# Kernel tuning notes

Hardware: AMD Instinct MI355X
Metric: run time of the kernel (lower is better)

Reference implementation:

```python
import jax, jax.numpy as jnp
import numpy as np

NUM_HEADS = 32
ROPE_BASE = 10000.0
MASK_NEG = -66504.0  # from (1 - tril) * -66504.0 in the source


def _rotate_half(x):
    d = x.shape[-1] // 2
    return jnp.concatenate([-x[..., d:], x[..., :d]], axis=-1)


def setup_inputs() -> dict:
    key = jax.random.key(0)
    k1, k2, k3, k4 = jax.random.split(key, 4)
    S, B, E = 2048, 2, 2048
    return {
        "hidden_states": jax.random.normal(k1, (S, B, E), dtype=jnp.float32) * 0.02,
        "qkv_w": jax.random.normal(k2, (E, 3 * E), dtype=jnp.float32) * 0.02,
        "qkv_b": jax.random.normal(k3, (3 * E,), dtype=jnp.float32) * 0.02,
        "out_w": jax.random.normal(k4, (E, E), dtype=jnp.float32) * 0.02,
        "out_b": jnp.zeros((E,), dtype=jnp.float32),
    }


def reference(hidden_states, qkv_w, qkv_b, out_w, out_b):
    # seq-first prompt/prefill path of IPEXTransformerAtten
    S, B, E = hidden_states.shape
    H = NUM_HEADS
    D = E // H

    # fused QKV projection (mm_qkv_out)
    qkv = jnp.einsum('sbe,ef->sbf', hidden_states, qkv_w) + qkv_b  # [S,B,3E]
    q, k, v = jnp.split(qkv, 3, axis=-1)
    q = q.reshape(S, B, H, D)
    k = k.reshape(S, B, H, D)
    v = v.reshape(S, B, H, D)

    # rotary embedding (GPT-NeoX style, full head_dim)
    inv_freq = 1.0 / (ROPE_BASE ** (jnp.arange(0, D, 2, dtype=jnp.float32) / D))
    freqs = jnp.arange(S, dtype=jnp.float32)[:, None] * inv_freq  # [S, D/2]
    emb = jnp.concatenate([freqs, freqs], axis=-1)  # [S, D]
    cos = jnp.cos(emb)[:, None, None, :].astype(hidden_states.dtype)
    sin = jnp.sin(emb)[:, None, None, :].astype(hidden_states.dtype)
    q = q * cos + _rotate_half(q) * sin
    k = k * cos + _rotate_half(k) * sin

    # scaled dot-product attention with causal mask
    scale = 1.0 / jnp.sqrt(jnp.array(D, dtype=hidden_states.dtype))
    scores = jnp.einsum('sbhd,tbhd->bhst', q, k) * scale  # [B,H,S,S]
    causal = jnp.tril(jnp.ones((S, S), dtype=scores.dtype))
    scores = scores + (1.0 - causal) * MASK_NEG
    attn = jax.nn.softmax(scores, axis=-1)
    ctx = jnp.einsum('bhst,tbhd->sbhd', attn, v).reshape(S, B, E)

    # output projection
    return jnp.einsum('sbe,ef->sbf', ctx, out_w) + out_b
```

## Files before the change

kernel.cpp:

```cpp
#include <hip/hip_runtime.h>
#include <hip/hip_bf16.h>

#define S_LEN 2048
#define BATCH 2
#define EMB   2048
#define NH    32
#define HD    64
#define M_ROWS (S_LEN * BATCH)
#define QKV_N  (3 * EMB)

typedef short bf16x8 __attribute__((ext_vector_type(8)));
typedef float f32x4  __attribute__((ext_vector_type(4)));

__device__ __forceinline__ unsigned short f2bf(float f) {
  unsigned int u = __float_as_uint(f);
  u += 0x7fffu + ((u >> 16) & 1u);
  return (unsigned short)(u >> 16);
}
__device__ __forceinline__ float bf2f(unsigned short h) {
  return __uint_as_float(((unsigned int)h) << 16);
}
__device__ __forceinline__ void async_copy16(const void* g, void* lds) {
  __builtin_amdgcn_global_load_lds(
      (const __attribute__((address_space(1))) void*)g,
      (__attribute__((address_space(3))) void*)lds, 16, 0, 0);
}

#if __has_builtin(__builtin_amdgcn_exp2f)
#define EXP2F(x) __builtin_amdgcn_exp2f(x)
#else
#define EXP2F(x) __expf((x) * 0.6931471805599453f)
#endif


__global__ __launch_bounds__(256) void cast_to_bf16(
    const float* __restrict__ in, unsigned short* __restrict__ out, int n4) {
  int i = blockIdx.x * 256 + threadIdx.x;
  if (i >= n4) return;
  float4 v = reinterpret_cast<const float4*>(in)[i];
  ushort4 o;
  o.x = f2bf(v.x); o.y = f2bf(v.y); o.z = f2bf(v.z); o.w = f2bf(v.w);
  reinterpret_cast<ushort4*>(out)[i] = o;
}

__global__ __launch_bounds__(256) void transpose_cast(
    const float* __restrict__ in, unsigned short* __restrict__ out, int R, int C) {
  __shared__ float tile[32][33];
  const int bc = blockIdx.x * 32, br = blockIdx.y * 32;
  const int tx = threadIdx.x & 31, ty = threadIdx.x >> 5;
  #pragma unroll
  for (int rr = ty; rr < 32; rr += 8)
    tile[rr][tx] = in[(size_t)(br + rr) * C + bc + tx];
  __syncthreads();
  #pragma unroll
  for (int rr = ty; rr < 32; rr += 8)
    out[(size_t)(bc + rr) * R + br + tx] = f2bf(tile[tx][rr]);
}


__global__ __launch_bounds__(256) void gemm_qkv(
    const unsigned short* __restrict__ A,
    const unsigned short* __restrict__ Wt,
    const float* __restrict__ bias,
    unsigned short* __restrict__ Qo,
    unsigned short* __restrict__ Ko,
    unsigned short* __restrict__ Vo) {
  __shared__ __align__(16) unsigned short As[128 * 64];
  __shared__ __align__(16) unsigned short Bs[128 * 64];
  const int tid = threadIdx.x;
  const int n0 = blockIdx.x * 128;
  const int m0 = blockIdx.y * 128;
  const int wave = tid >> 6, lane = tid & 63;
  const int wm = (wave >> 1) * 64, wn = (wave & 1) * 64;
  const int lm = lane & 15, lq = lane >> 4;
  const int K = 2048;

  const int srow = tid >> 3;
  const int gch  = (tid & 7) ^ (srow & 7);
  const unsigned short* Ab = A  + (size_t)(m0 + srow) * K + gch * 8;
  const unsigned short* Bb = Wt + (size_t)(n0 + srow) * K + gch * 8;

  f32x4 acc[4][4] = {};

  for (int k0 = 0; k0 < K; k0 += 64) {
    #pragma unroll
    for (int rep = 0; rep < 4; rep++) {
      async_copy16(Ab + (size_t)rep * 32 * K + k0, As + (size_t)(tid + 256 * rep) * 8);
      async_copy16(Bb + (size_t)rep * 32 * K + k0, Bs + (size_t)(tid + 256 * rep) * 8);
    }
    __syncthreads();
    #pragma unroll
    for (int ks = 0; ks < 2; ks++) {
      bf16x8 a[4], b[4];
      #pragma unroll
      for (int i = 0; i < 4; i++) {
        const int R = wm + i*16 + lm;
        a[i] = *reinterpret_cast<const bf16x8*>(
            As + (size_t)R * 64 + (((ks*4 + lq) ^ (R & 7)) * 8));
      }
      #pragma unroll
      for (int j = 0; j < 4; j++) {
        const int R = wn + j*16 + lm;
        b[j] = *reinterpret_cast<const bf16x8*>(
            Bs + (size_t)R * 64 + (((ks*4 + lq) ^ (R & 7)) * 8));
      }
      #pragma unroll
      for (int i = 0; i < 4; i++)
        #pragma unroll
        for (int j = 0; j < 4; j++)
          acc[i][j] = __builtin_amdgcn_mfma_f32_16x16x32_bf16(a[i], b[j], acc[i][j], 0, 0, 0);
    }
    __syncthreads();
  }

  const int which = n0 >> 11;
  unsigned short* dst = (which == 0) ? Qo : (which == 1) ? Ko : Vo;
  float bv[4];
  #pragma unroll
  for (int j = 0; j < 4; j++) bv[j] = bias[n0 + wn + j*16 + lm];

  if (which < 2) {
    #pragma unroll
    for (int j = 0; j < 2; j++) {
      const int n = n0 + wn + j*16 + lm;
      const int e = n & (EMB - 1), h = e >> 6, d = e & 63;
      const float invf = EXP2F((float)d * -0.4152410118609203f);
      #pragma unroll
      for (int i = 0; i < 4; i++) {
        #pragma unroll
        for (int r = 0; r < 4; r++) {
          const int m = m0 + wm + i*16 + lq*4 + r;
          const int s = m >> 1, b = m & 1;
          const float v1 = acc[i][j][r]   + bv[j];
          const float v2 = acc[i][j+2][r] + bv[j+2];
          float sn, cs;
          __sincosf((float)s * invf, &sn, &cs);
          const size_t base = (((size_t)b * NH + h) * S_LEN + s) * HD + d;
          dst[base]      = f2bf(v1 * cs - v2 * sn);
          dst[base + 32] = f2bf(v2 * cs + v1 * sn);
        }
      }
    }
  } else {
    #pragma unroll
    for (int j = 0; j < 4; j++) {
      const int n = n0 + wn + j*16 + lm;
      const int e = n & (EMB - 1), h = e >> 6, d = e & 63;
      #pragma unroll
      for (int i = 0; i < 4; i++) {
        #pragma unroll
        for (int r = 0; r < 4; r++) {
          const int m = m0 + wm + i*16 + lq*4 + r;
          const int s = m >> 1, b = m & 1;
          dst[(((size_t)b * NH + h) * S_LEN + s) * HD + d] = f2bf(acc[i][j][r] + bv[j]);
        }
      }
    }
  }
}


__global__ __launch_bounds__(256) void transpose_v(
    const unsigned short* __restrict__ V, unsigned short* __restrict__ VT) {
  __shared__ unsigned short t[64][65];
  const int bh = blockIdx.y;
  const int s0 = blockIdx.x * 64;
  const int tx = threadIdx.x & 63, ty = threadIdx.x >> 6;
  const unsigned short* src = V + ((size_t)bh * S_LEN + s0) * HD;
  #pragma unroll
  for (int r = ty; r < 64; r += 4)
    t[r][tx] = src[(size_t)r * HD + tx];
  __syncthreads();
  unsigned short* dst = VT + (size_t)bh * HD * S_LEN + s0;
  #pragma unroll
  for (int r = ty; r < 64; r += 4)
    dst[(size_t)r * S_LEN + tx] = t[tx][r];
}


__global__ __launch_bounds__(256) void attn_kernel(
    const unsigned short* __restrict__ Q,
    const unsigned short* __restrict__ K,
    const unsigned short* __restrict__ VT,
    unsigned short* __restrict__ ctx) {
  const int bh = blockIdx.x;
  const int p  = blockIdx.y;
  const int tid = threadIdx.x;
  const int wave = tid >> 6, lane = tid & 63;
  const int lm = lane & 15, lq = lane >> 4;
  const int b = bh >> 5, h = bh & 31;
  const char* Qb8 = (const char*)(Q  + (size_t)bh * S_LEN * HD);
  const char* Kb8 = (const char*)(K  + (size_t)bh * S_LEN * HD);
  const char* Vb8 = (const char*)(VT + (size_t)bh * HD * S_LEN);

  __shared__ __align__(16) unsigned short Ks[2][2][64][32];
  __shared__ __align__(16) unsigned short Vs[2][2][64][32];
  __shared__ __align__(16) unsigned short Pbuf[4][32][72];
  unsigned short* Pw = &Pbuf[wave][0][0];

  const float C = 0.18033688011112042f;
  const int q0A = p * 128, q0B = (15 - p) * 128;
  const int r0A = q0A + wave * 32, r0B = q0B + wave * 32;
  const int nt = (q0B >> 6) + 2;

  const int srw = tid >> 2, sc16 = (tid & 3) * 16;

  bf16x8 qf[2][2][2];
  #pragma unroll
  for (int s = 0; s < 2; s++) {
    const int rr = (s == 0) ? r0A : r0B;
    #pragma unroll
    for (int i = 0; i < 2; i++)
      #pragma unroll
      for (int ks = 0; ks < 2; ks++)
        qf[s][i][ks] = *reinterpret_cast<const bf16x8*>(
            Qb8 + (size_t)(rr + i*16 + lm) * 128 + ks*64 + lq*16);
  }

  f32x4 O[2][2][4] = {};
  float l[2][2][4] = {};

  {
    char* kd = (char*)&Ks[0][0][0][0];
    char* vd = (char*)&Vs[0][0][0][0];
    async_copy16(Kb8 + (size_t)srw * 128      + sc16, kd        + tid*16);
    async_copy16(Kb8 + (size_t)srw * 128 + 64 + sc16, kd + 4096 + tid*16);
    async_copy16(Vb8 + (size_t)srw * 4096      + sc16, vd        + tid*16);
    async_copy16(Vb8 + (size_t)srw * 4096 + 64 + sc16, vd + 4096 + tid*16);
  }
  __syncthreads();

  for (int t = 0; t < nt; t++) {
    const int t0 = t * 64;
    const int buf = t & 1;

    if (t + 1 < nt) {
      const int t1 = t0 + 64;
      char* kd = (char*)&Ks[buf ^ 1][0][0][0];
      char* vd = (char*)&Vs[buf ^ 1][0][0][0];
      async_copy16(Kb8 + (size_t)(t1 + srw) * 128      + sc16, kd        + tid*16);
      async_copy16(Kb8 + (size_t)(t1 + srw) * 128 + 64 + sc16, kd + 4096 + tid*16);
      async_copy16(Vb8 + (size_t)srw * 4096 + t1*2      + sc16, vd        + tid*16);
      async_copy16(Vb8 + (size_t)srw * 4096 + t1*2 + 64 + sc16, vd + 4096 + tid*16);
    }

    const char* KsB = (const char*)&Ks[buf][0][0][0];
    const char* VsB = (const char*)&Vs[buf][0][0][0];

    #pragma unroll
    for (int s = 0; s < 2; s++) {
      const int rr = (s == 0) ? r0A : r0B;
      if (t0 <= rr + 31) {
        const bool clean = (t0 + 63 <= rr);
        const int jmax  = clean ? 4 : ((rr == t0) ? 2 : 4);
        const int kslim = clean ? 2 : ((rr == t0) ? 1 : 2);
        const int srow_c = rr + lq * 4;

        f32x4 sc[2][4] = {};
        #pragma unroll
        for (int ks = 0; ks < 2; ks++) {
          bf16x8 kf[4];
          #pragma unroll
          for (int j = 0; j < 4; j++)
            if (j < jmax)
              kf[j] = *reinterpret_cast<const bf16x8*>(
                  KsB + ks*4096 + (j*16 + lm)*64 + lq*16);
          #pragma unroll
          for (int i = 0; i < 2; i++)
            #pragma unroll
            for (int j = 0; j < 4; j++)
              if (j < jmax)
                sc[i][j] = __builtin_amdgcn_mfma_f32_16x16x32_bf16(
                    qf[s][i][ks], kf[j], sc[i][j], 0, 0, 0);
        }

        if (clean) {
          #pragma unroll
          for (int i = 0; i < 2; i++)
            #pragma unroll
            for (int j = 0; j < 4; j++)
              #pragma unroll
              for (int r = 0; r < 4; r++) {
                const float pe = EXP2F(sc[i][j][r] * C);
                l[s][i][r] += pe;
                Pw[(i*16 + lq*4 + r) * 72 + j*16 + lm] = f2bf(pe);
              }
        } else {
          #pragma unroll
          for (int i = 0; i < 2; i++)
            #pragma unroll
            for (int j = 0; j < 4; j++)
              if (j < jmax)
                #pragma unroll
                for (int r = 0; r < 4; r++) {
                  const int srow = srow_c + i*16 + r;
                  const int tcol = t0 + j*16 + lm;
                  const float pe = (tcol <= srow) ? EXP2F(sc[i][j][r] * C) : 0.0f;
                  l[s][i][r] += pe;
                  Pw[(i*16 + lq*4 + r) * 72 + j*16 + lm] = f2bf(pe);
                }
        }

        #pragma unroll
        for (int ks = 0; ks < 2; ks++) {
          if (ks < kslim) {
            bf16x8 pf[2], vf[4];
            #pragma unroll
            for (int i = 0; i < 2; i++)
              pf[i] = *reinterpret_cast<const bf16x8*>(Pw + (i*16 + lm)*72 + ks*32 + lq*8);
            #pragma unroll
            for (int j = 0; j < 4; j++)
              vf[j] = *reinterpret_cast<const bf16x8*>(
                  VsB + ks*4096 + (j*16 + lm)*64 + lq*16);
            #pragma unroll
            for (int i = 0; i < 2; i++)
              #pragma unroll
              for (int j = 0; j < 4; j++)
                O[s][i][j] = __builtin_amdgcn_mfma_f32_16x16x32_bf16(
                    pf[i], vf[j], O[s][i][j], 0, 0, 0);
          }
        }
      }
    }
    __syncthreads();
  }

  #pragma unroll
  for (int s = 0; s < 2; s++) {
    const int rr = (s == 0) ? r0A : r0B;
    #pragma unroll
    for (int i = 0; i < 2; i++) {
      #pragma unroll
      for (int r = 0; r < 4; r++) {
        float sum = l[s][i][r];
        sum += __shfl_xor(sum, 1, 64);
        sum += __shfl_xor(sum, 2, 64);
        sum += __shfl_xor(sum, 4, 64);
        sum += __shfl_xor(sum, 8, 64);
        const float inv = 1.0f / sum;
        const int srow = rr + lq*4 + i*16 + r;
        #pragma unroll
        for (int j = 0; j < 4; j++) {
          const int d = j*16 + lm;
          ctx[((size_t)srow * BATCH + b) * EMB + h*HD + d] = f2bf(O[s][i][j][r] * inv);
        }
      }
    }
  }
}


__global__ __launch_bounds__(256) void gemm_out(
    const unsigned short* __restrict__ A,
    const unsigned short* __restrict__ Wt,
    const float* __restrict__ bias,
    float* __restrict__ out) {
  __shared__ __align__(16) unsigned short As[128 * 64];
  __shared__ __align__(16) unsigned short Bs[128 * 64];
  const int tid = threadIdx.x;
  const int n0 = blockIdx.x * 128;
  const int m0 = blockIdx.y * 128;
  const int wave = tid >> 6, lane = tid & 63;
  const int wm = (wave >> 1) * 64, wn = (wave & 1) * 64;
  const int lm = lane & 15, lq = lane >> 4;
  const int K = 2048;

  const int srow = tid >> 3;
  const int gch  = (tid & 7) ^ (srow & 7);
  const unsigned short* Ab = A  + (size_t)(m0 + srow) * K + gch * 8;
  const unsigned short* Bb = Wt + (size_t)(n0 + srow) * K + gch * 8;

  f32x4 acc[4][4] = {};

  for (int k0 = 0; k0 < K; k0 += 64) {
    #pragma unroll
    for (int rep = 0; rep < 4; rep++) {
      async_copy16(Ab + (size_t)rep * 32 * K + k0, As + (size_t)(tid + 256 * rep) * 8);
      async_copy16(Bb + (size_t)rep * 32 * K + k0, Bs + (size_t)(tid + 256 * rep) * 8);
    }
    __syncthreads();
    #pragma unroll
    for (int ks = 0; ks < 2; ks++) {
      bf16x8 a[4], b[4];
      #pragma unroll
      for (int i = 0; i < 4; i++) {
        const int R = wm + i*16 + lm;
        a[i] = *reinterpret_cast<const bf16x8*>(
            As + (size_t)R * 64 + (((ks*4 + lq) ^ (R & 7)) * 8));
      }
      #pragma unroll
      for (int j = 0; j < 4; j++) {
        const int R = wn + j*16 + lm;
        b[j] = *reinterpret_cast<const bf16x8*>(
            Bs + (size_t)R * 64 + (((ks*4 + lq) ^ (R & 7)) * 8));
      }
      #pragma unroll
      for (int i = 0; i < 4; i++)
        #pragma unroll
        for (int j = 0; j < 4; j++)
          acc[i][j] = __builtin_amdgcn_mfma_f32_16x16x32_bf16(a[i], b[j], acc[i][j], 0, 0, 0);
    }
    __syncthreads();
  }

  #pragma unroll
  for (int j = 0; j < 4; j++) {
    const int n = n0 + wn + j*16 + lm;
    const float bv = bias[n];
    #pragma unroll
    for (int i = 0; i < 4; i++) {
      #pragma unroll
      for (int r = 0; r < 4; r++) {
        const int m = m0 + wm + i*16 + lq*4 + r;
        out[(size_t)m * EMB + n] = acc[i][j][r] + bv;
      }
    }
  }
}


extern "C" void kernel_launch(void* const* d_in, const int* in_sizes, int n_in,
                              void* d_out, int out_size, void* d_ws, size_t ws_size,
                              hipStream_t stream) {
  const float* hidden = (const float*)d_in[0];
  const float* qkv_w  = (const float*)d_in[1];
  const float* qkv_b  = (const float*)d_in[2];
  const float* out_w  = (const float*)d_in[3];
  const float* out_b  = (const float*)d_in[4];
  float* out = (float*)d_out;

  unsigned short* ws = (unsigned short*)d_ws;
  unsigned short* hbf   = ws;
  unsigned short* qkvwT = hbf   + (size_t)M_ROWS * EMB;
  unsigned short* outwT = qkvwT + (size_t)QKV_N * EMB;
  unsigned short* Qb    = outwT + (size_t)EMB * EMB;
  unsigned short* Kb    = Qb    + (size_t)64 * S_LEN * HD;
  unsigned short* Vb    = Kb    + (size_t)64 * S_LEN * HD;
  unsigned short* VTb   = Vb    + (size_t)64 * S_LEN * HD;
  unsigned short* ctx   = VTb   + (size_t)64 * S_LEN * HD;

  cast_to_bf16<<<(M_ROWS * EMB / 4) / 256, 256, 0, stream>>>(hidden, hbf, M_ROWS * EMB / 4);
  transpose_cast<<<dim3(QKV_N / 32, EMB / 32), 256, 0, stream>>>(qkv_w, qkvwT, EMB, QKV_N);
  transpose_cast<<<dim3(EMB / 32, EMB / 32), 256, 0, stream>>>(out_w, outwT, EMB, EMB);

  gemm_qkv<<<dim3(QKV_N / 128, M_ROWS / 128), 256, 0, stream>>>(hbf, qkvwT, qkv_b, Qb, Kb, Vb);

  transpose_v<<<dim3(S_LEN / 64, 64), 256, 0, stream>>>(Vb, VTb);

  attn_kernel<<<dim3(64, 8), 256, 0, stream>>>(Qb, Kb, VTb, ctx);

  gemm_out<<<dim3(EMB / 128, M_ROWS / 128), 256, 0, stream>>>(ctx, outwT, out_b, out);
}
```

Before: 368.1 us.

## Halve attention query tile per block, double-buffer out GEMM, merge weight transposes

The attention kernel now gives each wave 16 query rows instead of 32 and launches twice as many blocks (64x16), still pairing a low and a high causal tile for load balance. This raises parallelism on the many-CU GPU and cuts per-wave registers, at the cost of reusing each K/V tile over fewer query rows. The output GEMM gains double-buffered LDS with async prefetch of the next K slice. The two weight transpose launches are merged into one 3D-grid launch.

```diff
diff --git a/kernel.cpp b/kernel.cpp
--- a/kernel.cpp
+++ b/kernel.cpp
@@ -43,10 +43,17 @@
   reinterpret_cast<ushort4*>(out)[i] = o;
 }
 
-__global__ __launch_bounds__(256) void transpose_cast(
-    const float* __restrict__ in, unsigned short* __restrict__ out, int R, int C) {
+__global__ __launch_bounds__(256) void transpose_cast2(
+    const float* __restrict__ qkv_w, const float* __restrict__ out_w,
+    unsigned short* __restrict__ qkvwT, unsigned short* __restrict__ outwT) {
   __shared__ float tile[32][33];
-  const int bc = blockIdx.x * 32, br = blockIdx.y * 32;
+  const int z = blockIdx.z;
+  const int C = z ? EMB : QKV_N;
+  const int bc = blockIdx.x * 32;
+  if (bc >= C) return;
+  const float* in = z ? out_w : qkv_w;
+  unsigned short* out = z ? outwT : qkvwT;
+  const int br = blockIdx.y * 32;
   const int tx = threadIdx.x & 31, ty = threadIdx.x >> 5;
   #pragma unroll
   for (int rr = ty; rr < 32; rr += 8)
@@ -54,7 +61,7 @@
   __syncthreads();
   #pragma unroll
   for (int rr = ty; rr < 32; rr += 8)
-    out[(size_t)(bc + rr) * R + br + tx] = f2bf(tile[tx][rr]);
+    out[(size_t)(bc + rr) * EMB + br + tx] = f2bf(tile[tx][rr]);
 }
 
 
@@ -195,30 +202,28 @@
 
   __shared__ __align__(16) unsigned short Ks[2][2][64][32];
   __shared__ __align__(16) unsigned short Vs[2][2][64][32];
-  __shared__ __align__(16) unsigned short Pbuf[4][32][72];
+  __shared__ __align__(16) unsigned short Pbuf[4][16][72];
   unsigned short* Pw = &Pbuf[wave][0][0];
 
   const float C = 0.18033688011112042f;
-  const int q0A = p * 128, q0B = (15 - p) * 128;
-  const int r0A = q0A + wave * 32, r0B = q0B + wave * 32;
-  const int nt = (q0B >> 6) + 2;
+  const int rA = p * 64 + wave * 16;
+  const int rB = (31 - p) * 64 + wave * 16;
+  const int nt = 32 - p;
 
   const int srw = tid >> 2, sc16 = (tid & 3) * 16;
 
-  bf16x8 qf[2][2][2];
+  bf16x8 qf[2][2];
   #pragma unroll
   for (int s = 0; s < 2; s++) {
-    const int rr = (s == 0) ? r0A : r0B;
-    #pragma unroll
-    for (int i = 0; i < 2; i++)
-      #pragma unroll
-      for (int ks = 0; ks < 2; ks++)
-        qf[s][i][ks] = *reinterpret_cast<const bf16x8*>(
-            Qb8 + (size_t)(rr + i*16 + lm) * 128 + ks*64 + lq*16);
-  }
-
-  f32x4 O[2][2][4] = {};
-  float l[2][2][4] = {};
+    const int rr = (s == 0) ? rA : rB;
+    #pragma unroll
+    for (int ks = 0; ks < 2; ks++)
+      qf[s][ks] = *reinterpret_cast<const bf16x8*>(
+          Qb8 + (size_t)(rr + lm) * 128 + ks*64 + lq*16);
+  }
+
+  f32x4 O[2][4] = {};
+  float l[2][4] = {};
 
   {
     char* kd = (char*)&Ks[0][0][0][0];
@@ -249,14 +254,13 @@
 
     #pragma unroll
     for (int s = 0; s < 2; s++) {
-      const int rr = (s == 0) ? r0A : r0B;
-      if (t0 <= rr + 31) {
+      const int rr = (s == 0) ? rA : rB;
+      if (t0 <= rr + 15) {
         const bool clean = (t0 + 63 <= rr);
-        const int jmax  = clean ? 4 : ((rr == t0) ? 2 : 4);
-        const int kslim = clean ? 2 : ((rr == t0) ? 1 : 2);
-        const int srow_c = rr + lq * 4;
-
-        f32x4 sc[2][4] = {};
+        const int jmax = clean ? 4 : min(4, ((rr + 15 - t0) >> 4) + 1);
+        const int kslim = (jmax + 1) >> 1;
+
+        f32x4 sc[4] = {};
         #pragma unroll
         for (int ks = 0; ks < 2; ks++) {
           bf16x8 kf[4];
@@ -266,58 +270,53 @@
               kf[j] = *reinterpret_cast<const bf16x8*>(
                   KsB + ks*4096 + (j*16 + lm)*64 + lq*16);
           #pragma unroll
-          for (int i = 0; i < 2; i++)
-            #pragma unroll
-            for (int j = 0; j < 4; j++)
-              if (j < jmax)
-                sc[i][j] = __builtin_amdgcn_mfma_f32_16x16x32_bf16(
-                    qf[s][i][ks], kf[j], sc[i][j], 0, 0, 0);
+          for (int j = 0; j < 4; j++)
+            if (j < jmax)
+              sc[j] = __builtin_amdgcn_mfma_f32_16x16x32_bf16(
+                  qf[s][ks], kf[j], sc[j], 0, 0, 0);
         }
 
         if (clean) {
           #pragma unroll
-          for (int i = 0; i < 2; i++)
+          for (int j = 0; j < 4; j++)
             #pragma unroll
-            for (int j = 0; j < 4; j++)
+            for (int r = 0; r < 4; r++) {
+              const float pe = EXP2F(sc[j][r] * C);
+              l[s][r] += pe;
+              Pw[(lq*4 + r) * 72 + j*16 + lm] = f2bf(pe);
+            }
+        } else {
+          #pragma unroll
+          for (int j = 0; j < 4; j++)
+            if (j < jmax)
               #pragma unroll
               for (int r = 0; r < 4; r++) {
-                const float pe = EXP2F(sc[i][j][r] * C);
-                l[s][i][r] += pe;
-                Pw[(i*16 + lq*4 + r) * 72 + j*16 + lm] = f2bf(pe);
+                const int srow = rr + lq*4 + r;
+                const int tcol = t0 + j*16 + lm;
+                const float pe = (tcol <= srow) ? EXP2F(sc[j][r] * C) : 0.0f;
+                l[s][r] += pe;
+                Pw[(lq*4 + r) * 72 + j*16 + lm] = f2bf(pe);
               }
-        } else {
-          #pragma unroll
-          for (int i = 0; i < 2; i++)
+          if (jmax & 1) {
             #pragma unroll
-            for (int j = 0; j < 4; j++)
-              if (j < jmax)
-                #pragma unroll
-                for (int r = 0; r < 4; r++) {
-                  const int srow = srow_c + i*16 + r;
-                  const int tcol = t0 + j*16 + lm;
-                  const float pe = (tcol <= srow) ? EXP2F(sc[i][j][r] * C) : 0.0f;
-                  l[s][i][r] += pe;
-                  Pw[(i*16 + lq*4 + r) * 72 + j*16 + lm] = f2bf(pe);
-                }
+            for (int r = 0; r < 4; r++)
+              Pw[(lq*4 + r) * 72 + jmax*16 + lm] = 0;
+          }
         }
 
         #pragma unroll
         for (int ks = 0; ks < 2; ks++) {
           if (ks < kslim) {
-            bf16x8 pf[2], vf[4];
-            #pragma unroll
-            for (int i = 0; i < 2; i++)
-              pf[i] = *reinterpret_cast<const bf16x8*>(Pw + (i*16 + lm)*72 + ks*32 + lq*8);
+            bf16x8 pf = *reinterpret_cast<const bf16x8*>(Pw + lm*72 + ks*32 + lq*8);
+            bf16x8 vf[4];
             #pragma unroll
             for (int j = 0; j < 4; j++)
               vf[j] = *reinterpret_cast<const bf16x8*>(
                   VsB + ks*4096 + (j*16 + lm)*64 + lq*16);
             #pragma unroll
-            for (int i = 0; i < 2; i++)
-              #pragma unroll
-              for (int j = 0; j < 4; j++)
-                O[s][i][j] = __builtin_amdgcn_mfma_f32_16x16x32_bf16(
-                    pf[i], vf[j], O[s][i][j], 0, 0, 0);
+            for (int j = 0; j < 4; j++)
+              O[s][j] = __builtin_amdgcn_mfma_f32_16x16x32_bf16(
+                  pf, vf[j], O[s][j], 0, 0, 0);
           }
         }
       }
@@ -327,23 +326,20 @@
 
   #pragma unroll
   for (int s = 0; s < 2; s++) {
-    const int rr = (s == 0) ? r0A : r0B;
-    #pragma unroll
-    for (int i = 0; i < 2; i++) {
-      #pragma unroll
-      for (int r = 0; r < 4; r++) {
-        float sum = l[s][i][r];
-        sum += __shfl_xor(sum, 1, 64);
-        sum += __shfl_xor(sum, 2, 64);
-        sum += __shfl_xor(sum, 4, 64);
-        sum += __shfl_xor(sum, 8, 64);
-        const float inv = 1.0f / sum;
-        const int srow = rr + lq*4 + i*16 + r;
-        #pragma unroll
-        for (int j = 0; j < 4; j++) {
-          const int d = j*16 + lm;
-          ctx[((size_t)srow * BATCH + b) * EMB + h*HD + d] = f2bf(O[s][i][j][r] * inv);
-        }
+    const int rr = (s == 0) ? rA : rB;
+    #pragma unroll
+    for (int r = 0; r < 4; r++) {
+      float sum = l[s][r];
+      sum += __shfl_xor(sum, 1, 64);
+      sum += __shfl_xor(sum, 2, 64);
+      sum += __shfl_xor(sum, 4, 64);
+      sum += __shfl_xor(sum, 8, 64);
+      const float inv = 1.0f / sum;
+      const int srow = rr + lq*4 + r;
+      #pragma unroll
+      for (int j = 0; j < 4; j++) {
+        const int d = j*16 + lm;
+        ctx[((size_t)srow * BATCH + b) * EMB + h*HD + d] = f2bf(O[s][j][r] * inv);
       }
     }
   }
@@ -355,8 +351,8 @@
     const unsigned short* __restrict__ Wt,
     const float* __restrict__ bias,
     float* __restrict__ out) {
-  __shared__ __align__(16) unsigned short As[128 * 64];
-  __shared__ __align__(16) unsigned short Bs[128 * 64];
+  __shared__ __align__(16) unsigned short As[2][128 * 64];
+  __shared__ __align__(16) unsigned short Bs[2][128 * 64];
   const int tid = threadIdx.x;
   const int n0 = blockIdx.x * 128;
   const int m0 = blockIdx.y * 128;
@@ -372,13 +368,23 @@
 
   f32x4 acc[4][4] = {};
 
-  for (int k0 = 0; k0 < K; k0 += 64) {
-    #pragma unroll
-    for (int rep = 0; rep < 4; rep++) {
-      async_copy16(Ab + (size_t)rep * 32 * K + k0, As + (size_t)(tid + 256 * rep) * 8);
-      async_copy16(Bb + (size_t)rep * 32 * K + k0, Bs + (size_t)(tid + 256 * rep) * 8);
-    }
-    __syncthreads();
+  #pragma unroll
+  for (int rep = 0; rep < 4; rep++) {
+    async_copy16(Ab + (size_t)rep * 32 * K, As[0] + (size_t)(tid + 256 * rep) * 8);
+    async_copy16(Bb + (size_t)rep * 32 * K, Bs[0] + (size_t)(tid + 256 * rep) * 8);
+  }
+  __syncthreads();
+
+  for (int kt = 0; kt < 32; kt++) {
+    const int buf = kt & 1;
+    if (kt + 1 < 32) {
+      const int k1 = (kt + 1) * 64;
+      #pragma unroll
+      for (int rep = 0; rep < 4; rep++) {
+        async_copy16(Ab + (size_t)rep * 32 * K + k1, As[buf ^ 1] + (size_t)(tid + 256 * rep) * 8);
+        async_copy16(Bb + (size_t)rep * 32 * K + k1, Bs[buf ^ 1] + (size_t)(tid + 256 * rep) * 8);
+      }
+    }
     #pragma unroll
     for (int ks = 0; ks < 2; ks++) {
       bf16x8 a[4], b[4];
@@ -386,13 +392,13 @@
       for (int i = 0; i < 4; i++) {
         const int R = wm + i*16 + lm;
         a[i] = *reinterpret_cast<const bf16x8*>(
-            As + (size_t)R * 64 + (((ks*4 + lq) ^ (R & 7)) * 8));
+            As[buf] + (size_t)R * 64 + (((ks*4 + lq) ^ (R & 7)) * 8));
       }
       #pragma unroll
       for (int j = 0; j < 4; j++) {
         const int R = wn + j*16 + lm;
         b[j] = *reinterpret_cast<const bf16x8*>(
-            Bs + (size_t)R * 64 + (((ks*4 + lq) ^ (R & 7)) * 8));
+            Bs[buf] + (size_t)R * 64 + (((ks*4 + lq) ^ (R & 7)) * 8));
       }
       #pragma unroll
       for (int i = 0; i < 4; i++)
@@ -440,14 +446,13 @@
   unsigned short* ctx   = VTb   + (size_t)64 * S_LEN * HD;
 
   cast_to_bf16<<<(M_ROWS * EMB / 4) / 256, 256, 0, stream>>>(hidden, hbf, M_ROWS * EMB / 4);
-  transpose_cast<<<dim3(QKV_N / 32, EMB / 32), 256, 0, stream>>>(qkv_w, qkvwT, EMB, QKV_N);
-  transpose_cast<<<dim3(EMB / 32, EMB / 32), 256, 0, stream>>>(out_w, outwT, EMB, EMB);
+  transpose_cast2<<<dim3(QKV_N / 32, EMB / 32, 2), 256, 0, stream>>>(qkv_w, out_w, qkvwT, outwT);
 
   gemm_qkv<<<dim3(QKV_N / 128, M_ROWS / 128), 256, 0, stream>>>(hbf, qkvwT, qkv_b, Qb, Kb, Vb);
 
   transpose_v<<<dim3(S_LEN / 64, 64), 256, 0, stream>>>(Vb, VTb);
 
-  attn_kernel<<<dim3(64, 8), 256, 0, stream>>>(Qb, Kb, VTb, ctx);
+  attn_kernel<<<dim3(64, 16), 256, 0, stream>>>(Qb, Kb, VTb, ctx);
 
   gemm_out<<<dim3(EMB / 128, M_ROWS / 128), 256, 0, stream>>>(ctx, outwT, out_b, out);
 }
```

Measured after the change: 420.0 us. 1.14x slower.
